# Kernel optimization log

Hardware: AMD Instinct MI355X
Metric: run time of the kernel (lower is better)

The kernel has to match this reference:

```python
import jax, jax.numpy as jnp
import numpy as np

# Module constants (from GaussRenderer.__init__ with image 128x128)
H = 128
W = 128
TS = 64          # TILE_SIZE
P_MAX = 2048
WHITE_BKGD = True
TH, TW = H // TS, W // TS
NT = TH * TW     # num_tiles


def _tile_grids():
    th, tw = jnp.meshgrid(jnp.arange(TH), jnp.arange(TW), indexing='ij')
    h_mins = (th * TS).reshape(-1).astype(jnp.float32)   # [NT]
    w_mins = (tw * TS).reshape(-1).astype(jnp.float32)   # [NT]
    lx = jnp.arange(TS, dtype=jnp.float32)
    xx, yy = jnp.meshgrid(lx, lx, indexing='xy')         # xx[i,j]=j, yy[i,j]=i
    local = jnp.stack([xx, yy], axis=-1).reshape(TS * TS, 2)
    # tile_coords[t, p] = (x, y) global pixel coordinate
    coords = local[None, :, :] + jnp.stack([w_mins, h_mins], axis=-1)[:, None, :]
    return h_mins, w_mins, coords


def setup_inputs() -> dict:
    key = jax.random.key(0)
    k1, k2, k3, k4, k5 = jax.random.split(key, 5)
    N = 100000
    means2D = jax.random.uniform(k1, (N, 2), dtype=jnp.float32) * jnp.array([float(W), float(H)], dtype=jnp.float32)
    A = jax.random.normal(k2, (N, 2, 2), dtype=jnp.float32) * 2.0
    cov2d = A @ jnp.swapaxes(A, 1, 2) + 0.5 * jnp.eye(2, dtype=jnp.float32)  # SPD
    color = jax.random.uniform(k3, (N, 3), dtype=jnp.float32)
    opacity = jax.random.uniform(k4, (N, 1), dtype=jnp.float32)
    depths = jax.random.uniform(k5, (N,), dtype=jnp.float32) * 10.0 + 0.2
    return {"means2D": means2D, "cov2d": cov2d, "color": color, "opacity": opacity, "depths": depths}


def _render(means2D, cov2d, color, opacity, depths):
    h_mins, w_mins, tile_coords = _tile_grids()
    h_maxs = h_mins + (TS - 1.0)
    w_maxs = w_mins + (TS - 1.0)

    # --- get_radius / get_rect (torch.no_grad -> stop_gradient) ---
    c = jax.lax.stop_gradient(cov2d)
    det = c[:, 0, 0] * c[:, 1, 1] - c[:, 0, 1] * c[:, 1, 0]
    mid = 0.5 * (c[:, 0, 0] + c[:, 1, 1])
    s = jnp.sqrt(jnp.clip(mid ** 2 - det, 0.1, None))
    radii = 3.0 * jnp.ceil(jnp.sqrt(jnp.maximum(mid + s, mid - s)))  # [N]
    m = jax.lax.stop_gradient(means2D)
    rmin = m - radii[:, None]
    rmax = m + radii[:, None]
    rmin = jnp.stack([jnp.clip(rmin[:, 0], 0.0, W - 1.0), jnp.clip(rmin[:, 1], 0.0, H - 1.0)], axis=-1)
    rmax = jnp.stack([jnp.clip(rmax[:, 0], 0.0, W - 1.0), jnp.clip(rmax[:, 1], 0.0, H - 1.0)], axis=-1)

    # --- tile/gaussian overlap test ---
    ov_x = jnp.minimum(rmax[None, :, 0], w_maxs[:, None]) > jnp.maximum(rmin[None, :, 0], w_mins[:, None])
    ov_y = jnp.minimum(rmax[None, :, 1], h_maxs[:, None]) > jnp.maximum(rmin[None, :, 1], h_mins[:, None])
    overlap = ov_x & ov_y                                   # [NT, N]

    # --- per-tile depth sort, keep front-most P_MAX ---
    FAR = jnp.float32(1e10)
    d_tiled = jnp.where(overlap, depths[None, :], FAR)      # [NT, N]
    idx = jnp.argsort(d_tiled, axis=1)[:, :P_MAX]           # [NT, P]
    sd = jnp.take_along_axis(d_tiled, idx, axis=1)          # sorted depths
    valid = (sd < 1e9).astype(means2D.dtype)                # [NT, P]

    sm = means2D[idx]          # [NT, P, 2]
    sc = cov2d[idx]            # [NT, P, 2, 2]
    so = opacity[idx][..., 0]  # [NT, P]
    scol = color[idx]          # [NT, P, 3]

    # --- conic (inverse 2x2 covariance) ---
    a_ = sc[..., 0, 0]; b_ = sc[..., 0, 1]; c2_ = sc[..., 1, 0]; d_ = sc[..., 1, 1]
    inv_det = 1.0 / jnp.clip(a_ * d_ - b_ * c2_, 1e-6, None)
    c00 = d_ * inv_det; c01 = -b_ * inv_det; c10 = -c2_ * inv_det; c11 = a_ * inv_det

    # --- per-pixel gaussian weights: [NT, TS*TS, P] ---
    dx0 = tile_coords[:, :, None, 0] - sm[:, None, :, 0]
    dx1 = tile_coords[:, :, None, 1] - sm[:, None, :, 1]
    gw = jnp.exp(-0.5 * (dx0 * dx0 * c00[:, None, :] + dx1 * dx1 * c11[:, None, :]
                         + dx0 * dx1 * (c01 + c10)[:, None, :]))

    # --- front-to-back alpha compositing ---
    alpha = jnp.minimum(gw * so[:, None, :], 0.99) * valid[:, None, :]
    T = jnp.cumprod(jnp.concatenate([jnp.ones_like(alpha[:, :, :1]), 1.0 - alpha[:, :, :-1]], axis=2), axis=2)
    w = alpha * T                                           # [NT, TS*TS, P]
    acc = w.sum(axis=2)                                     # [NT, TS*TS]
    tcol = jnp.einsum('tpn,tnc->tpc', w, scol)              # [NT, TS*TS, 3]
    if WHITE_BKGD:
        tcol = tcol + (1.0 - acc)[..., None]
    tdep = (w * sd[:, None, :]).sum(axis=2)

    # --- untile ---
    render_color = tcol.reshape(TH, TW, TS, TS, 3).transpose(0, 2, 1, 3, 4).reshape(H, W, 3)
    render_depth = tdep.reshape(TH, TW, TS, TS).transpose(0, 2, 1, 3).reshape(H, W, 1)
    render_alpha = acc.reshape(TH, TW, TS, TS).transpose(0, 2, 1, 3).reshape(H, W, 1)
    return render_color, render_depth, render_alpha


def reference(means2D, cov2d, color, opacity, depths):
    return _render(means2D, cov2d, color, opacity, depths)
```

## Files before the change

kernel.cpp:

```cpp
#include <hip/hip_runtime.h>

#define IMG 128
#define TSZ 64
#define NTILES 4
#define PMAX 2048
#define NHIST 4096
#define CAP 64
#define NCHUNK 16
#define CHUNK 128
#define QCH 32
#define NPIX 4096
#define NPSEG 16
#define PLANE ((size_t)NTILES * NCHUNK * NPIX)
#define NTHR 256
#define RUNITS (NTILES * NCHUNK * NPSEG)
#define POISON 0xAAAAAAAAu
#define LOG2E 1.4426950408889634f

typedef unsigned short u16;
typedef unsigned int uint32;
typedef unsigned long long u64;


__device__ __forceinline__ uint32 dbucket(float d) {
    int b = (int)(d * 256.0f);
    return (uint32)min(max(b, 0), NHIST - 1);
}

__device__ __forceinline__ void gauss_rect(const float* means, const float* cov,
                                           int i, float& rminx, float& rminy,
                                           float& rmaxx, float& rmaxy) {
    const float4 cv = ((const float4*)cov)[i];
    float det = cv.x * cv.w - cv.y * cv.z;
    float mid = 0.5f * (cv.x + cv.w);
    float s = sqrtf(fmaxf(mid * mid - det, 0.1f));
    float radius = 3.0f * ceilf(sqrtf(fmaxf(mid + s, mid - s)));
    const float2 m = ((const float2*)means)[i];
    rminx = fminf(fmaxf(m.x - radius, 0.f), (float)(IMG - 1));
    rmaxx = fminf(fmaxf(m.x + radius, 0.f), (float)(IMG - 1));
    rminy = fminf(fmaxf(m.y - radius, 0.f), (float)(IMG - 1));
    rmaxy = fminf(fmaxf(m.y + radius, 0.f), (float)(IMG - 1));
}

__device__ __forceinline__ bool tile_overlap(int t, float rminx, float rminy,
                                             float rmaxx, float rmaxy) {
    float wmin = (float)((t & 1) * TSZ), hmin = (float)((t >> 1) * TSZ);
    float wmax = wmin + (float)(TSZ - 1), hmax = hmin + (float)(TSZ - 1);
    return (fminf(rmaxx, wmax) > fmaxf(rminx, wmin)) &&
           (fminf(rmaxy, hmax) > fmaxf(rminy, hmin));
}

__global__ __launch_bounds__(NTHR) void k_pre2(
        const float* __restrict__ means, const float* __restrict__ cov,
        const float* __restrict__ depths, uint32* __restrict__ cnt,
        u64* __restrict__ slots, int N) {
    int i = blockIdx.x * NTHR + threadIdx.x;
    if (i >= N) return;
    float rminx, rminy, rmaxx, rmaxy;
    gauss_rect(means, cov, i, rminx, rminy, rmaxx, rmaxy);
    float d = depths[i];
    uint32 b = dbucket(d);
    u64 key = ((u64)__float_as_uint(d) << 32) | (uint32)i;
    #pragma unroll
    for (int t = 0; t < NTILES; t++) {
        if (tile_overlap(t, rminx, rminy, rmaxx, rmaxy)) {
            uint32 slot = atomicAdd(&cnt[t * NHIST + b], 1u) - POISON;
            if (slot < CAP)
                slots[((size_t)t * NHIST + b) * CAP + slot] = key;
        }
    }
}

__global__ __launch_bounds__(NTHR) void k_rank4(const uint32* __restrict__ cnt,
        const u64* __restrict__ slots,
        const float* __restrict__ means, const float* __restrict__ cov,
        const float* __restrict__ color, const float* __restrict__ opac,
        float* __restrict__ params) {
    const int wq = blockIdx.x * (NTHR / 64) + (threadIdx.x >> 6);
    const int tile = wq >> 12, b = wq & (NHIST - 1);
    const int lane = threadIdx.x & 63;
    const uint32* cn = cnt + (size_t)tile * NHIST;
    uint32 n = min(cn[b] - POISON, (uint32)CAP);
    if (!n && b != NHIST - 1) return;
    uint32 base = 0;
    for (int j0 = 0; j0 < b; j0 += 64) {
        int j = j0 + lane;
        uint32 c = (j < b) ? min(cn[j] - POISON, (uint32)CAP) : 0u;
        #pragma unroll
        for (int dlt = 1; dlt < 64; dlt <<= 1)
            c += __shfl_xor(c, dlt, 64);
        base += c;
        if (base >= PMAX) break;
    }
    if (base >= PMAX) return;
    if (b == NHIST - 1) {
        for (uint32 p = base + n + (uint32)lane; p < PMAX; p += 64) {
            float4 z0 = {0.f, 0.f, 0.f, 0.f};
            float4 z1 = {0.f, -1e30f, 0.f, 0.f};
            float4* P = (float4*)(params + ((size_t)tile * PMAX + p) * 12);
            P[0] = z0; P[1] = z1; P[2] = z0;
        }
        if (!n) return;
    }
    const u64* S = slots + ((size_t)tile * NHIST + b) * CAP;
    u64 ki = (lane < (int)n) ? S[lane] : ~0ull;
    uint32 r = base;
    for (uint32 j = 0; j < n; j++) {
        u64 kj = __shfl(ki, (int)j, 64);
        r += (kj < ki) ? 1u : 0u;
    }
    if (lane < (int)n && r < PMAX) {
        uint32 idx = (uint32)(ki & 0xffffffffu);
        const float4 cv = ((const float4*)cov)[idx];
        const float2 mn = ((const float2*)means)[idx];
        float invdet = 1.0f / fmaxf(cv.x * cv.w - cv.y * cv.z, 1e-6f);
        const float k = -0.5f * LOG2E;
        float4 p0, p1, p2;
        p0.x = mn.x; p0.y = mn.y;
        p0.z = k * cv.w * invdet;
        p0.w = k * cv.x * invdet;
        p1.x = -k * (cv.y + cv.z) * invdet;
        p1.y = log2f(opac[idx]);
        p1.z = color[3*idx]; p1.w = color[3*idx+1];
        p2.x = color[3*idx+2];
        p2.y = __uint_as_float((uint32)(ki >> 32));
        p2.z = 0.f; p2.w = 0.f;
        float4* P = (float4*)(params + ((size_t)tile * PMAX + r) * 12);
        P[0] = p0; P[1] = p1; P[2] = p2;
    }
}

__global__ __launch_bounds__(NTHR, 4) void k_render(
        const float* __restrict__ params, float* __restrict__ partials) {
    __shared__ __align__(16) float4 gp[CHUNK * 3];
    const int unit = blockIdx.x, tid = threadIdx.x;
    const int tile  = unit >> 8;
    const int chunk = (unit >> 4) & 15;
    const int pseg  = unit & 15;
    const float4* src = (const float4*)(params + ((size_t)tile * PMAX + (size_t)chunk * CHUNK) * 12);
    for (int j = tid; j < CHUNK * 3; j += NTHR) gp[j] = src[j];
    __syncthreads();
    const int p = pseg * NTHR + tid;
    const float px = (float)((tile & 1) * TSZ + (p & 63));
    const float py = (float)((tile >> 1) * TSZ + (p >> 6));
    float Tc[4], cr[4], cg[4], cb[4], dp[4], ac[4];
    #pragma unroll
    for (int s = 0; s < 4; s++) {
        Tc[s] = 1.f; cr[s] = 0.f; cg[s] = 0.f; cb[s] = 0.f; dp[s] = 0.f; ac[s] = 0.f;
    }
    #pragma unroll 2
    for (int g = 0; g < QCH; g++) {
        #pragma unroll
        for (int s = 0; s < 4; s++) {
            const int gg = s * QCH + g;
            float4 q0 = gp[3*gg], q1 = gp[3*gg+1], q2 = gp[3*gg+2];
            float dx = px - q0.x, dy = py - q0.y;
            float pw = fmaf(dx*dx, q0.z, q1.y);
            pw = fmaf(dy*dy, q0.w, pw);
            pw = fmaf(dx*dy, q1.x, pw);
            float al = fminf(exp2f(pw), 0.99f);
            float w = al * Tc[s];
            cr[s] += w * q1.z; cg[s] += w * q1.w; cb[s] += w * q2.x;
            dp[s] += w * q2.y; ac[s] += w;
            Tc[s] *= (1.f - al);
        }
    }
    float T = 1.f, fr = 0.f, fg = 0.f, fb = 0.f, fd = 0.f, fa = 0.f;
    #pragma unroll
    for (int s = 0; s < 4; s++) {
        fr += T * cr[s]; fg += T * cg[s]; fb += T * cb[s];
        fd += T * dp[s]; fa += T * ac[s];
        T *= Tc[s];
    }
    size_t base = ((size_t)tile * NCHUNK + chunk) * NPIX + (size_t)p;
    partials[0*PLANE + base] = T;
    partials[1*PLANE + base] = fr;
    partials[2*PLANE + base] = fg;
    partials[3*PLANE + base] = fb;
    partials[4*PLANE + base] = fd;
    partials[5*PLANE + base] = fa;
}

__global__ __launch_bounds__(NTHR) void k_combine(
        const float* __restrict__ partials, float* __restrict__ out) {
    int q = blockIdx.x * NTHR + threadIdx.x;
    int tile = q >> 12, p = q & (NPIX - 1);
    float T = 1.f, cr = 0.f, cg = 0.f, cb = 0.f, dep = 0.f, acc = 0.f;
    #pragma unroll
    for (int c = 0; c < NCHUNK; c++) {
        size_t base = ((size_t)tile * NCHUNK + c) * NPIX + (size_t)p;
        float Tk = partials[0*PLANE + base];
        cr  += T * partials[1*PLANE + base];
        cg  += T * partials[2*PLANE + base];
        cb  += T * partials[3*PLANE + base];
        dep += T * partials[4*PLANE + base];
        acc += T * partials[5*PLANE + base];
        T *= Tk;
    }
    int gx = (tile & 1) * TSZ + (p & 63);
    int gy = (tile >> 1) * TSZ + (p >> 6);
    int pix = gy * IMG + gx;
    float wb = 1.f - acc;
    out[3*pix+0] = cr + wb;
    out[3*pix+1] = cg + wb;
    out[3*pix+2] = cb + wb;
    out[IMG*IMG*3 + pix] = dep;
    out[IMG*IMG*4 + pix] = acc;
}

extern "C" void kernel_launch(void* const* d_in, const int* in_sizes, int n_in,
                              void* d_out, int out_size, void* d_ws, size_t ws_size,
                              hipStream_t stream) {
    const float* means  = (const float*)d_in[0];
    const float* cov    = (const float*)d_in[1];
    const float* color  = (const float*)d_in[2];
    const float* opac   = (const float*)d_in[3];
    const float* depths = (const float*)d_in[4];
    int N = in_sizes[4];

    char* ws = (char*)d_ws;
    size_t off = 0;
    uint32* cnt        = (uint32*)(ws + off); off += (size_t)NTILES * NHIST * 4;
    u64*    slots      = (u64*)(ws + off);    off += (size_t)NTILES * NHIST * CAP * 8;
    float*  params     = (float*)(ws + off);  off += (size_t)NTILES * PMAX * 12 * 4;
    float*  partials   = (float*)(ws + off);  off += 6 * PLANE * 4;
    float*  out        = (float*)d_out;

    k_pre2<<<(N + NTHR - 1) / NTHR, NTHR, 0, stream>>>(means, cov, depths,
                                                       cnt, slots, N);
    k_rank4<<<(NTILES * NHIST) / (NTHR / 64), NTHR, 0, stream>>>(cnt, slots,
                                                                 means, cov,
                                                                 color, opac,
                                                                 params);
    k_render<<<RUNITS, NTHR, 0, stream>>>(params, partials);
    k_combine<<<(NTILES * NPIX) / NTHR, NTHR, 0, stream>>>(partials, out);
}
```

Before: 108.0 us.

## Skip far Gaussians per row via bound, repack params, restructure combine

Precomputes a per-Gaussian row bound (the maximum of the exponent over x for a given dy, plus log opacity) and skips the full evaluation when it falls below a cutoff where alpha is negligible. The parameter layout is repacked so the cheap row test needs only the first float4 from shared memory. The combine kernel now loads the partials cooperatively through shared memory, with 16 threads per block doing the per-pixel chain. The skip drops contributions below about 2^-23, which changes results slightly, and branching adds divergence within a wavefront.

```diff
diff --git a/kernel.cpp b/kernel.cpp
--- a/kernel.cpp
+++ b/kernel.cpp
@@ -16,6 +16,7 @@
 #define RUNITS (NTILES * NCHUNK * NPSEG)
 #define POISON 0xAAAAAAAAu
 #define LOG2E 1.4426950408889634f
+#define SKIPCUT -23.0f
 
 typedef unsigned short u16;
 typedef unsigned int uint32;
@@ -95,10 +96,10 @@
     if (base >= PMAX) return;
     if (b == NHIST - 1) {
         for (uint32 p = base + n + (uint32)lane; p < PMAX; p += 64) {
-            float4 z0 = {0.f, 0.f, 0.f, 0.f};
-            float4 z1 = {0.f, -1e30f, 0.f, 0.f};
+            float4 z0 = {0.f, 0.f, 0.f, -1e30f};
+            float4 zz = {0.f, 0.f, 0.f, 0.f};
             float4* P = (float4*)(params + ((size_t)tile * PMAX + p) * 12);
-            P[0] = z0; P[1] = z1; P[2] = z0;
+            P[0] = z0; P[1] = zz; P[2] = zz;
         }
         if (!n) return;
     }
@@ -115,16 +116,14 @@
         const float2 mn = ((const float2*)means)[idx];
         float invdet = 1.0f / fmaxf(cv.x * cv.w - cv.y * cv.z, 1e-6f);
         const float k = -0.5f * LOG2E;
+        float cA = k * cv.w * invdet;
+        float cB = k * cv.x * invdet;
+        float cC = -k * (cv.y + cv.z) * invdet;
+        float bnd = cB - (cC * cC) / (4.0f * cA);
         float4 p0, p1, p2;
-        p0.x = mn.x; p0.y = mn.y;
-        p0.z = k * cv.w * invdet;
-        p0.w = k * cv.x * invdet;
-        p1.x = -k * (cv.y + cv.z) * invdet;
-        p1.y = log2f(opac[idx]);
-        p1.z = color[3*idx]; p1.w = color[3*idx+1];
-        p2.x = color[3*idx+2];
-        p2.y = __uint_as_float((uint32)(ki >> 32));
-        p2.z = 0.f; p2.w = 0.f;
+        p0.x = mn.x; p0.y = mn.y; p0.z = bnd; p0.w = log2f(opac[idx]);
+        p1.x = cA;   p1.y = cB;   p1.z = cC;  p1.w = __uint_as_float((uint32)(ki >> 32));
+        p2.x = color[3*idx]; p2.y = color[3*idx+1]; p2.z = color[3*idx+2]; p2.w = 0.f;
         float4* P = (float4*)(params + ((size_t)tile * PMAX + r) * 12);
         P[0] = p0; P[1] = p1; P[2] = p2;
     }
@@ -153,16 +152,21 @@
         #pragma unroll
         for (int s = 0; s < 4; s++) {
             const int gg = s * QCH + g;
-            float4 q0 = gp[3*gg], q1 = gp[3*gg+1], q2 = gp[3*gg+2];
-            float dx = px - q0.x, dy = py - q0.y;
-            float pw = fmaf(dx*dx, q0.z, q1.y);
-            pw = fmaf(dy*dy, q0.w, pw);
-            pw = fmaf(dx*dy, q1.x, pw);
-            float al = fminf(exp2f(pw), 0.99f);
-            float w = al * Tc[s];
-            cr[s] += w * q1.z; cg[s] += w * q1.w; cb[s] += w * q2.x;
-            dp[s] += w * q2.y; ac[s] += w;
-            Tc[s] *= (1.f - al);
+            float4 q0 = gp[3*gg];
+            float dy = py - q0.y;
+            float t = fmaf(dy*dy, q0.z, q0.w);
+            if (t >= SKIPCUT) {
+                float4 q1 = gp[3*gg+1], q2 = gp[3*gg+2];
+                float dx = px - q0.x;
+                float pw = fmaf(dx*dx, q1.x, q0.w);
+                pw = fmaf(dy*dy, q1.y, pw);
+                pw = fmaf(dx*dy, q1.z, pw);
+                float al = fminf(exp2f(pw), 0.99f);
+                float w = al * Tc[s];
+                cr[s] += w * q2.x; cg[s] += w * q2.y; cb[s] += w * q2.z;
+                dp[s] += w * q1.w; ac[s] += w;
+                Tc[s] *= (1.f - al);
+            }
         }
     }
     float T = 1.f, fr = 0.f, fg = 0.f, fb = 0.f, fd = 0.f, fa = 0.f;
@@ -181,31 +185,41 @@
     partials[5*PLANE + base] = fa;
 }
 
-__global__ __launch_bounds__(NTHR) void k_combine(
+__global__ __launch_bounds__(NTHR) void k_combine2(
         const float* __restrict__ partials, float* __restrict__ out) {
-    int q = blockIdx.x * NTHR + threadIdx.x;
-    int tile = q >> 12, p = q & (NPIX - 1);
-    float T = 1.f, cr = 0.f, cg = 0.f, cb = 0.f, dep = 0.f, acc = 0.f;
-    #pragma unroll
-    for (int c = 0; c < NCHUNK; c++) {
-        size_t base = ((size_t)tile * NCHUNK + c) * NPIX + (size_t)p;
-        float Tk = partials[0*PLANE + base];
-        cr  += T * partials[1*PLANE + base];
-        cg  += T * partials[2*PLANE + base];
-        cb  += T * partials[3*PLANE + base];
-        dep += T * partials[4*PLANE + base];
-        acc += T * partials[5*PLANE + base];
-        T *= Tk;
-    }
-    int gx = (tile & 1) * TSZ + (p & 63);
-    int gy = (tile >> 1) * TSZ + (p >> 6);
-    int pix = gy * IMG + gx;
-    float wb = 1.f - acc;
-    out[3*pix+0] = cr + wb;
-    out[3*pix+1] = cg + wb;
-    out[3*pix+2] = cb + wb;
-    out[IMG*IMG*3 + pix] = dep;
-    out[IMG*IMG*4 + pix] = acc;
+    __shared__ float sv[6][NTHR];
+    const int blk = blockIdx.x, tid = threadIdx.x;
+    const int tile = blk >> 8;
+    const int p0 = (blk & 255) << 4;
+    const int ch = tid >> 4, pl = tid & 15;
+    size_t base = ((size_t)tile * NCHUNK + ch) * NPIX + (size_t)(p0 + pl);
+    #pragma unroll
+    for (int j = 0; j < 6; j++) sv[j][tid] = partials[(size_t)j * PLANE + base];
+    __syncthreads();
+    if (tid < 16) {
+        const int pp = p0 + tid;
+        float T = 1.f, cr = 0.f, cg = 0.f, cb = 0.f, dep = 0.f, acc = 0.f;
+        #pragma unroll
+        for (int c = 0; c < NCHUNK; c++) {
+            int idx = c * 16 + tid;
+            float Tk = sv[0][idx];
+            cr  += T * sv[1][idx];
+            cg  += T * sv[2][idx];
+            cb  += T * sv[3][idx];
+            dep += T * sv[4][idx];
+            acc += T * sv[5][idx];
+            T *= Tk;
+        }
+        int gx = (tile & 1) * TSZ + (pp & 63);
+        int gy = (tile >> 1) * TSZ + (pp >> 6);
+        int pix = gy * IMG + gx;
+        float wb = 1.f - acc;
+        out[3*pix+0] = cr + wb;
+        out[3*pix+1] = cg + wb;
+        out[3*pix+2] = cb + wb;
+        out[IMG*IMG*3 + pix] = dep;
+        out[IMG*IMG*4 + pix] = acc;
+    }
 }
 
 extern "C" void kernel_launch(void* const* d_in, const int* in_sizes, int n_in,
@@ -233,5 +247,5 @@
                                                                  color, opac,
                                                                  params);
     k_render<<<RUNITS, NTHR, 0, stream>>>(params, partials);
-    k_combine<<<(NTILES * NPIX) / NTHR, NTHR, 0, stream>>>(partials, out);
-}
+    k_combine2<<<NTILES * 256, NTHR, 0, stream>>>(partials, out);
+}
```

Measured after the change: 105.6 us. 2.2% less time.
